# Performance work log

Measured on AMD Instinct MI355X. Metric: run time of the kernel, lower is better.

## Reference

```python
import jax, jax.numpy as jnp
import numpy as np

B, S, D, E = 4, 4096, 1024, 8
TOP_K = 2


def setup_inputs() -> dict:
    key = jax.random.key(0)
    k_x, k_gw, k_gb, k_ew, k_eb = jax.random.split(key, 5)
    x = jax.random.normal(k_x, (B, S, D), dtype=jnp.float32)
    gate_w = jax.random.normal(k_gw, (E, D), dtype=jnp.float32) * 0.02
    gate_b = jax.random.normal(k_gb, (E,), dtype=jnp.float32) * 0.02
    expert_w = jax.random.normal(k_ew, (E, D, D), dtype=jnp.float32) * 0.02
    expert_b = jax.random.normal(k_eb, (E, D), dtype=jnp.float32) * 0.02
    return {"x": x, "gate_w": gate_w, "gate_b": gate_b,
            "expert_w": expert_w, "expert_b": expert_b}


def reference(x, gate_w, gate_b, expert_w, expert_b):
    b, s, d = x.shape
    h = x.reshape(-1, d)                                  # [T, D]
    # router: linear -> softmax (fp32) -> top-k -> renormalize
    router_logits = h @ gate_w.T + gate_b                 # [T, E]
    probs = jax.nn.softmax(router_logits.astype(jnp.float32), axis=-1)
    topw, sel = jax.lax.top_k(probs, TOP_K)               # [T, K]
    topw = topw / jnp.sum(topw, axis=-1, keepdims=True)
    topw = topw.astype(h.dtype)
    out = jnp.zeros_like(h)
    for e in range(E):  # small fixed loop over experts
        # per-token combine weight for expert e (0 if not selected)
        we = jnp.sum(jnp.where(sel == e, topw, 0.0), axis=-1)  # [T]
        out = out + (h @ expert_w[e].T + expert_b[e]) * we[:, None]
    return out.reshape(b, s, d), router_logits
```

## Files before the change

kernel.cpp:

```cpp
#include <hip/hip_runtime.h>
#include <hip/hip_bf16.h>

typedef unsigned short u16;
typedef unsigned int u32;

#define T_TOK 16384
#define DIM   1024
#define NEXP  8

#define XB_OFF      0
#define WB_OFF      33554432
#define CNT_OFF     50331648
#define LIST_OFF    50332160
#define SELW_OFF    50856448
#define CONTRIB_OFF 51380736
#define WS_NEED     118489600ULL

__device__ __forceinline__ u16 f2bf(float f) {
    u32 u = __float_as_uint(f);
    u += 0x7fff + ((u >> 16) & 1);
    return (u16)(u >> 16);
}
__device__ __forceinline__ float bf2f(u16 u) {
    return __uint_as_float(((u32)u) << 16);
}

__global__ __launch_bounds__(128) void k_zero(int* counts) {
    if (threadIdx.x < NEXP * 16) counts[threadIdx.x] = 0;
}

#define RT_PB 32

__global__ __launch_bounds__(256) void k_router(
    const float* __restrict__ x, const float* __restrict__ gw,
    const float* __restrict__ gb, float* __restrict__ logits,
    u16* __restrict__ xb, int* __restrict__ counts,
    int* __restrict__ lists, float4* __restrict__ selw,
    const float* __restrict__ ew, u16* __restrict__ wb)
{
    const int tid  = threadIdx.x;
    const int lane = tid & 63;
    const int w    = tid >> 6;

    __shared__ int   s_sel0[RT_PB], s_sel1[RT_PB];
    __shared__ int   s_lcnt[NEXP], s_gbase[NEXP];

    if (tid < NEXP) s_lcnt[tid] = 0;

    for (int i = 0; i < 8; ++i) {
        const int l = w * 8 + i;
        const int t = blockIdx.x * RT_PB + l;

        const float* xr = x + (size_t)t * DIM;
        float4 xs[4];
#pragma unroll
        for (int j = 0; j < 4; ++j)
            xs[j] = *reinterpret_cast<const float4*>(xr + (j * 64 + lane) * 4);

        float acc[NEXP];
#pragma unroll
        for (int e = 0; e < NEXP; ++e) {
            const float* gr = gw + e * DIM;
            float s = 0.f;
#pragma unroll
            for (int j = 0; j < 4; ++j) {
                float4 g = *reinterpret_cast<const float4*>(gr + (j * 64 + lane) * 4);
                s += xs[j].x * g.x + xs[j].y * g.y + xs[j].z * g.z + xs[j].w * g.w;
            }
            acc[e] = s;
        }
#pragma unroll
        for (int off = 1; off < 64; off <<= 1) {
#pragma unroll
            for (int e = 0; e < NEXP; ++e) acc[e] += __shfl_xor(acc[e], off);
        }
#pragma unroll
        for (int e = 0; e < NEXP; ++e) acc[e] += gb[e];

        int i0 = 0; float v0 = acc[0];
#pragma unroll
        for (int e = 1; e < NEXP; ++e) if (acc[e] > v0) { v0 = acc[e]; i0 = e; }
        int i1 = -1; float v1 = -3.4e38f;
#pragma unroll
        for (int e = 0; e < NEXP; ++e) if (e != i0 && acc[e] > v1) { v1 = acc[e]; i1 = e; }
        float e1  = __expf(v1 - v0);
        float inv = 1.f / (1.f + e1);
        float w0 = inv, w1 = e1 * inv;

        u16* xrow = xb + (size_t)t * DIM;
#pragma unroll
        for (int j = 0; j < 4; ++j) {
            int c = (j * 64 + lane) * 4;
            float4 v = xs[j];
            ushort4 u;
            u.x = f2bf(v.x); u.y = f2bf(v.y); u.z = f2bf(v.z); u.w = f2bf(v.w);
            *reinterpret_cast<ushort4*>(xrow + c) = u;
        }
        if (lane == 0) {
            float4 lo = make_float4(acc[0], acc[1], acc[2], acc[3]);
            float4 hi = make_float4(acc[4], acc[5], acc[6], acc[7]);
            *reinterpret_cast<float4*>(logits + (size_t)t * NEXP)     = lo;
            *reinterpret_cast<float4*>(logits + (size_t)t * NEXP + 4) = hi;
            selw[t] = make_float4(__int_as_float(i0), __int_as_float(i1), w0, w1);
            s_sel0[l] = i0; s_sel1[l] = i1;
        }
    }
    __syncthreads();

    int i0 = 0, i1 = 0, r0 = 0, r1 = 0;
    if (tid < RT_PB) {
        i0 = s_sel0[tid]; i1 = s_sel1[tid];
        r0 = atomicAdd(&s_lcnt[i0], 1);
        r1 = atomicAdd(&s_lcnt[i1], 1);
    }
    __syncthreads();
    if (tid < NEXP)
        s_gbase[tid] = atomicAdd(&counts[tid * 16], s_lcnt[tid]);
    __syncthreads();
    if (tid < RT_PB) {
        int t  = blockIdx.x * RT_PB + tid;
        lists[i0 * T_TOK + s_gbase[i0] + r0] = t * 2;
        lists[i1 * T_TOK + s_gbase[i1] + r1] = t * 2 + 1;
    }

    const int n4 = NEXP * DIM * DIM / 4;
    const int stride = gridDim.x * 256;
    for (int i = blockIdx.x * 256 + tid; i < n4; i += stride) {
        float4 v = reinterpret_cast<const float4*>(ew)[i];
        ushort4 u;
        u.x = f2bf(v.x); u.y = f2bf(v.y); u.z = f2bf(v.z); u.w = f2bf(v.w);
        reinterpret_cast<ushort4*>(wb)[i] = u;
    }
}


typedef __attribute__((ext_vector_type(8))) short bf16x8;
typedef __attribute__((ext_vector_type(4))) float f32x4;

#define GLDS16(g, l) __builtin_amdgcn_global_load_lds( \
    (const __attribute__((address_space(1))) void*)(g), \
    (__attribute__((address_space(3))) void*)(l), 16, 0, 0)

#define BAR() __builtin_amdgcn_s_barrier()
#define PRIO1() __builtin_amdgcn_s_setprio(1)
#define PRIO0() __builtin_amdgcn_s_setprio(0)
#define VMW0() asm volatile("s_waitcnt vmcnt(0)" ::: "memory")

template<int ATOMIC>
__global__ __launch_bounds__(256, 4) void k_gemm(
    const u16* __restrict__ xb, const u16* __restrict__ wb,
    const int* __restrict__ counts, const int* __restrict__ lists,
    const float4* __restrict__ selw, u16* __restrict__ contrib,
    float* __restrict__ out)
{
    __shared__ u16 lds[16384];

    const int bid = (blockIdx.x & 7) * 1024 + (blockIdx.x >> 3);
    const int e   = bid >> 10;
    const int mt  = (bid >> 3) & 127;
    const int nt  = bid & 7;
    const int cnt = counts[e * 16];
    if (mt * 128 >= cnt) return;

    const int tid  = threadIdx.x;
    const int lane = tid & 63;
    const int wid  = tid >> 6;
    const int wm   = wid >> 1;
    const int wn   = wid & 1;
    const int listbase = e * T_TOK;

    const int srow = tid >> 2;
    const int cA   = (((tid & 3) - (tid >> 3)) & 3) * 8;
    int tokA[2];
#pragma unroll
    for (int l = 0; l < 2; ++l) {
        int slot = mt * 128 + l * 64 + srow;
        tokA[l] = lists[listbase + (slot < cnt ? slot : cnt - 1)] >> 1;
    }
    const u16* srcA0 = xb + (size_t)tokA[0] * DIM + cA;
    const u16* srcA1 = xb + (size_t)tokA[1] * DIM + cA;
    const u16* srcB0 = wb + ((size_t)e << 20) + (size_t)(nt * 128 + srow) * DIM + cA;
    const u16* srcB1 = srcB0 + (size_t)64 * DIM;

#define STAGE(b, kk) do { \
    GLDS16(srcA0 + (kk), &lds[(b) * 8192 + wid * 512]); \
    GLDS16(srcA1 + (kk), &lds[(b) * 8192 + 2048 + wid * 512]); \
    GLDS16(srcB0 + (kk), &lds[(b) * 8192 + 4096 + wid * 512]); \
    GLDS16(srcB1 + (kk), &lds[(b) * 8192 + 4096 + 2048 + wid * 512]); } while (0)

    const int cs8  = (((lane >> 4) + ((lane >> 1) & 3)) & 3) * 8;
    const int offA = (wm * 64 + (lane & 15)) * 32 + cs8;
    const int offB = 4096 + (wn * 64 + (lane & 15)) * 32 + cs8;

    bf16x8 Af[4], Bf[4];
    f32x4 acc[4][4];
#pragma unroll
    for (int mi = 0; mi < 4; ++mi)
#pragma unroll
        for (int ni = 0; ni < 4; ++ni) acc[mi][ni] = (f32x4)0.f;

#define LDA4(b) do { \
    Af[0] = *(const bf16x8*)&lds[(b) * 8192 + 0 * 512 + offA]; \
    Af[1] = *(const bf16x8*)&lds[(b) * 8192 + 1 * 512 + offA]; \
    Af[2] = *(const bf16x8*)&lds[(b) * 8192 + 2 * 512 + offA]; \
    Af[3] = *(const bf16x8*)&lds[(b) * 8192 + 3 * 512 + offA]; } while (0)
#define LDB4(b) do { \
    Bf[0] = *(const bf16x8*)&lds[(b) * 8192 + 0 * 512 + offB]; \
    Bf[1] = *(const bf16x8*)&lds[(b) * 8192 + 1 * 512 + offB]; \
    Bf[2] = *(const bf16x8*)&lds[(b) * 8192 + 2 * 512 + offB]; \
    Bf[3] = *(const bf16x8*)&lds[(b) * 8192 + 3 * 512 + offB]; } while (0)
#define MFMA_ROW(i) do { \
    acc[i][0] = __builtin_amdgcn_mfma_f32_16x16x32_bf16(Af[i], Bf[0], acc[i][0], 0, 0, 0); \
    acc[i][1] = __builtin_amdgcn_mfma_f32_16x16x32_bf16(Af[i], Bf[1], acc[i][1], 0, 0, 0); \
    acc[i][2] = __builtin_amdgcn_mfma_f32_16x16x32_bf16(Af[i], Bf[2], acc[i][2], 0, 0, 0); \
    acc[i][3] = __builtin_amdgcn_mfma_f32_16x16x32_bf16(Af[i], Bf[3], acc[i][3], 0, 0, 0); } while (0)
#define MFMA16() do { MFMA_ROW(0); MFMA_ROW(1); MFMA_ROW(2); MFMA_ROW(3); } while (0)

    STAGE(0, 0);
    VMW0(); BAR();

    for (int s = 0; s < 31; ++s) {
        const int b = s & 1, nb = b ^ 1;
        STAGE(nb, (s + 1) * 32);
        LDA4(b); LDB4(b);
        PRIO1(); MFMA16(); PRIO0();
        VMW0(); BAR();
    }
    {
        LDA4(1); LDB4(1);
        PRIO1(); MFMA16(); PRIO0();
    }

    const int rbase = (lane >> 4) * 4;
    const int cbase = nt * 128 + wn * 64 + (lane & 15);
#pragma unroll
    for (int mi = 0; mi < 4; ++mi) {
#pragma unroll
        for (int r = 0; r < 4; ++r) {
            int slot = mt * 128 + wm * 64 + mi * 16 + rbase + r;
            if (slot < cnt) {
                int lv = lists[listbase + slot];
                if (ATOMIC) {
                    int tok = lv >> 1;
                    float4 sw = selw[tok];
                    float wgt = (lv & 1) ? sw.w : sw.z;
                    float* orow = out + (size_t)tok * DIM + cbase;
#pragma unroll
                    for (int ni = 0; ni < 4; ++ni)
                        atomicAdd(orow + ni * 16, acc[mi][ni][r] * wgt);
                } else {
                    u16* crow = contrib + (size_t)lv * DIM + cbase;
#pragma unroll
                    for (int ni = 0; ni < 4; ++ni)
                        crow[ni * 16] = f2bf(acc[mi][ni][r]);
                }
            }
        }
    }
}

__global__ __launch_bounds__(256) void k_combine(
    const u16* __restrict__ contrib, const float4* __restrict__ selw,
    const float* __restrict__ eb, float* __restrict__ out)
{
    const int lane = threadIdx.x & 63;
    const int t    = blockIdx.x * 4 + (threadIdx.x >> 6);
    float4 sw = selw[t];
    const int e0 = __float_as_int(sw.x);
    const int e1 = __float_as_int(sw.y);
    const float w0 = sw.z, w1 = sw.w;
    const u16* c0 = contrib + (size_t)(t * 2) * DIM;
    const u16* c1 = c0 + DIM;
    const float* b0 = eb + e0 * DIM;
    const float* b1 = eb + e1 * DIM;
    float* orow = out + (size_t)t * DIM;
#pragma unroll
    for (int j = 0; j < 2; ++j) {
        const int c = (j * 64 + lane) * 8;
        uint4 u0 = *reinterpret_cast<const uint4*>(c0 + c);
        uint4 u1 = *reinterpret_cast<const uint4*>(c1 + c);
        const u16* p0 = (const u16*)&u0;
        const u16* p1 = (const u16*)&u1;
#pragma unroll
        for (int h = 0; h < 2; ++h) {
            float4 bb0 = *reinterpret_cast<const float4*>(b0 + c + h * 4);
            float4 bb1 = *reinterpret_cast<const float4*>(b1 + c + h * 4);
            float4 o;
            o.x = w0 * (bf2f(p0[h*4+0]) + bb0.x) + w1 * (bf2f(p1[h*4+0]) + bb1.x);
            o.y = w0 * (bf2f(p0[h*4+1]) + bb0.y) + w1 * (bf2f(p1[h*4+1]) + bb1.y);
            o.z = w0 * (bf2f(p0[h*4+2]) + bb0.z) + w1 * (bf2f(p1[h*4+2]) + bb1.z);
            o.w = w0 * (bf2f(p0[h*4+3]) + bb0.w) + w1 * (bf2f(p1[h*4+3]) + bb1.w);
            *reinterpret_cast<float4*>(orow + c + h * 4) = o;
        }
    }
}

__global__ __launch_bounds__(256) void k_bias(
    const float4* __restrict__ selw, const float* __restrict__ eb,
    float* __restrict__ out)
{
    const int lane = threadIdx.x & 63;
    const int t    = blockIdx.x * 4 + (threadIdx.x >> 6);
    float4 sw = selw[t];
    const float* b0 = eb + __float_as_int(sw.x) * DIM;
    const float* b1 = eb + __float_as_int(sw.y) * DIM;
    float* orow = out + (size_t)t * DIM;
#pragma unroll
    for (int j = 0; j < 4; ++j) {
        int c = (j * 64 + lane) * 4;
        float4 f0 = *reinterpret_cast<const float4*>(b0 + c);
        float4 f1 = *reinterpret_cast<const float4*>(b1 + c);
        float4 o;
        o.x = sw.z * f0.x + sw.w * f1.x;
        o.y = sw.z * f0.y + sw.w * f1.y;
        o.z = sw.z * f0.z + sw.w * f1.z;
        o.w = sw.z * f0.w + sw.w * f1.w;
        *reinterpret_cast<float4*>(orow + c) = o;
    }
}

extern "C" void kernel_launch(void* const* d_in, const int* in_sizes, int n_in,
                              void* d_out, int out_size, void* d_ws, size_t ws_size,
                              hipStream_t stream) {
    const float* x  = (const float*)d_in[0];
    const float* gw = (const float*)d_in[1];
    const float* gb = (const float*)d_in[2];
    const float* ew = (const float*)d_in[3];
    const float* eb = (const float*)d_in[4];

    float* out    = (float*)d_out;
    float* logits = out + (size_t)T_TOK * DIM;

    char*   ws      = (char*)d_ws;
    u16*    xb      = (u16*)(ws + XB_OFF);
    u16*    wb      = (u16*)(ws + WB_OFF);
    int*    counts  = (int*)(ws + CNT_OFF);
    int*    lists   = (int*)(ws + LIST_OFF);
    float4* selw    = (float4*)(ws + SELW_OFF);
    u16*    contrib = (u16*)(ws + CONTRIB_OFF);

    k_zero<<<1, 128, 0, stream>>>(counts);
    k_router<<<T_TOK / RT_PB, 256, 0, stream>>>(x, gw, gb, logits, xb, counts,
                                                lists, selw, ew, wb);

    const int grid = NEXP * 128 * 8;
    if (ws_size >= WS_NEED) {
        k_gemm<0><<<grid, 256, 0, stream>>>(xb, wb, counts, lists, selw, contrib, out);
        k_combine<<<T_TOK / 4, 256, 0, stream>>>(contrib, selw, eb, out);
    } else {
        k_bias<<<T_TOK / 4, 256, 0, stream>>>(selw, eb, out);
        k_gemm<1><<<grid, 256, 0, stream>>>(xb, wb, counts, lists, selw, contrib, out);
    }
}
```

Measured before the change: 162.4 us.

## Triple-buffer GEMM K-loop with staggered K start and partial vmcnt waits

The expert GEMM moves from a double-buffered LDS pipeline with full vmcnt(0) waits to a three-stage ring buffer. It prefetches two K-steps ahead and waits with vmcnt(4), so one stage's global-to-LDS loads stay in flight during compute. Each block also starts its K loop at a different rotated offset, so that concurrent blocks spread their reads across memory. LDS grows from 32 KB to 48 KB and the launch-bounds occupancy hint drops from 4 to 3 blocks. Separately, the zeroing kernel is replaced by hipMemsetAsync.

```diff
diff --git a/kernel.cpp b/kernel.cpp
--- a/kernel.cpp
+++ b/kernel.cpp
@@ -23,10 +23,6 @@
 }
 __device__ __forceinline__ float bf2f(u16 u) {
     return __uint_as_float(((u32)u) << 16);
-}
-
-__global__ __launch_bounds__(128) void k_zero(int* counts) {
-    if (threadIdx.x < NEXP * 16) counts[threadIdx.x] = 0;
 }
 
 #define RT_PB 32
@@ -144,16 +140,17 @@
 #define BAR() __builtin_amdgcn_s_barrier()
 #define PRIO1() __builtin_amdgcn_s_setprio(1)
 #define PRIO0() __builtin_amdgcn_s_setprio(0)
+#define VMW4() asm volatile("s_waitcnt vmcnt(4)" ::: "memory")
 #define VMW0() asm volatile("s_waitcnt vmcnt(0)" ::: "memory")
 
 template<int ATOMIC>
-__global__ __launch_bounds__(256, 4) void k_gemm(
+__global__ __launch_bounds__(256, 3) void k_gemm(
     const u16* __restrict__ xb, const u16* __restrict__ wb,
     const int* __restrict__ counts, const int* __restrict__ lists,
     const float4* __restrict__ selw, u16* __restrict__ contrib,
     float* __restrict__ out)
 {
-    __shared__ u16 lds[16384];
+    __shared__ u16 lds[24576];
 
     const int bid = (blockIdx.x & 7) * 1024 + (blockIdx.x >> 3);
     const int e   = bid >> 10;
@@ -168,6 +165,8 @@
     const int wm   = wid >> 1;
     const int wn   = wid & 1;
     const int listbase = e * T_TOK;
+
+    const int s0 = ((int)(blockIdx.x >> 3) * 11) & 31;
 
     const int srow = tid >> 2;
     const int cA   = (((tid & 3) - (tid >> 3)) & 3) * 8;
@@ -216,20 +215,25 @@
     acc[i][3] = __builtin_amdgcn_mfma_f32_16x16x32_bf16(Af[i], Bf[3], acc[i][3], 0, 0, 0); } while (0)
 #define MFMA16() do { MFMA_ROW(0); MFMA_ROW(1); MFMA_ROW(2); MFMA_ROW(3); } while (0)
 
-    STAGE(0, 0);
-    VMW0(); BAR();
-
-    for (int s = 0; s < 31; ++s) {
-        const int b = s & 1, nb = b ^ 1;
-        STAGE(nb, (s + 1) * 32);
-        LDA4(b); LDB4(b);
-        PRIO1(); MFMA16(); PRIO0();
-        VMW0(); BAR();
-    }
-    {
-        LDA4(1); LDB4(1);
-        PRIO1(); MFMA16(); PRIO0();
-    }
+#define PHASE(p, b, sb) do { \
+    if ((p) < 30) STAGE(sb, ((s0 + (p) + 2) & 31) * 32); \
+    LDA4(b); LDB4(b); \
+    PRIO1(); MFMA16(); PRIO0(); \
+    if ((p) < 30) { VMW4(); } else { VMW0(); } \
+    if ((p) < 31) BAR(); \
+} while (0)
+
+    STAGE(0, (s0 & 31) * 32);
+    STAGE(1, ((s0 + 1) & 31) * 32);
+    VMW4(); BAR();
+
+    for (int j = 0; j < 10; ++j) {
+        PHASE(j * 3 + 0, 0, 2);
+        PHASE(j * 3 + 1, 1, 0);
+        PHASE(j * 3 + 2, 2, 1);
+    }
+    PHASE(30, 0, 2);
+    PHASE(31, 1, 0);
 
     const int rbase = (lane >> 4) * 4;
     const int cbase = nt * 128 + wn * 64 + (lane & 15);
@@ -339,7 +343,7 @@
     float4* selw    = (float4*)(ws + SELW_OFF);
     u16*    contrib = (u16*)(ws + CONTRIB_OFF);
 
-    k_zero<<<1, 128, 0, stream>>>(counts);
+    hipMemsetAsync((void*)(ws + CNT_OFF), 0, 512, stream);
     k_router<<<T_TOK / RT_PB, 256, 0, stream>>>(x, gw, gb, logits, xb, counts,
                                                 lists, selw, ew, wb);
 
```

Measured after the change: 162.5 us. Within noise of the previous version (+0.0%).
